# Kernel optimization log

Measured on AMD Instinct MI355X. Metric: run time of the kernel, lower is better.

## Reference

```python
import jax, jax.numpy as jnp
import numpy as np

INF = 1e10
PROBS_THRESHOLD = 0.7
ALPHA = 3.0
DICE_EPS = 1e-6


def edt2d(mask0):
    """Exact Euclidean distance transform of a 2D slice.
    mask0: [H, W] bool, True where the pixel is background (value == 0).
    Returns per-pixel distance to nearest background pixel (0 on background),
    matching scipy.ndimage.distance_transform_edt on the complementary image.
    Separable decomposition: 1D column pass then min-plus row pass.
    """
    H, W = mask0.shape
    ii = jnp.arange(H, dtype=jnp.float32)
    # column pass: g[i, j] = min_{i': mask0[i', j]} |i - i'|   -> [H, W]
    d_col = jnp.abs(ii[:, None] - ii[None, :])                 # [H(i), H(i')]
    g = jnp.min(jnp.where(mask0[None, :, :], d_col[:, :, None], INF), axis=1)
    jj = jnp.arange(W, dtype=jnp.float32)
    dj2 = (jj[:, None] - jj[None, :]) ** 2                     # [W(j), W(j')]
    # row pass: edt^2[i, j] = min_{j'} g[i, j']^2 + (j - j')^2
    edt2 = jnp.min(g[:, None, :] ** 2 + dj2[None, :, :], axis=2)  # [H, W]
    return jnp.sqrt(edt2)


def _combined_distance(y_threshed):
    """y_threshed: [B, 1, D, H, W] float 0/1. Returns combined clipped EDT map."""
    x = y_threshed[:, 0]                                        # [B, D, H, W]
    B, D, H, W = x.shape
    edt_slices = jax.vmap(jax.vmap(lambda s, v: edt2d(s == v), in_axes=(0, None)),
                          in_axes=(0, None))
    dst = edt_slices(x, 1.0)   # distance_transform_edt(slice): bg where slice==0
    inv = edt_slices(x, 0.0)   # wait: see below
    # scipy edt(img): nonzero pixels -> dist to nearest zero => background mask is img==0
    # so dst uses mask0 = (s == 0); inverted uses mask0 = (1 - s == 0) i.e. (s == 1)
    dst = jax.vmap(jax.vmap(lambda s: edt2d(s == 0.0)))(x)      # [B, D, H, W]
    inv = jax.vmap(jax.vmap(lambda s: edt2d(s == 1.0)))(x)      # [B, D, H, W]
    combined = dst + inv
    # get_glioma_indices: first/last slice containing foreground
    present = jnp.any(x > 0, axis=(2, 3))                       # [B, D]
    first = jnp.argmax(present, axis=1)                         # [B]
    last = D - 1 - jnp.argmax(present[:, ::-1], axis=1)         # [B]
    dvec = jnp.arange(D)
    in_range = (dvec[None, :] >= first[:, None]) & (dvec[None, :] <= last[:, None])
    combined = jnp.where(in_range[:, :, None, None], combined, 0.0)
    # thresh_mode == 'max': thresh_val = max of dst of the LAST processed slice
    dst_last = jax.vmap(lambda d, l: d[l])(dst, last)           # [B, H, W]
    thresh = jnp.max(dst_last, axis=(1, 2))                     # [B]
    combined = jnp.minimum(combined, thresh[:, None, None, None])
    return combined[:, None]                                    # [B, 1, D, H, W]


def dice_coefficient(y_pred, y_true):
    inter = jnp.sum(y_pred * y_true)
    return (2.0 * inter) / (jnp.sum(y_pred) + jnp.sum(y_true) + DICE_EPS)


def reference(y_pred, y_true):
    y_threshed = jax.lax.stop_gradient((y_pred > PROBS_THRESHOLD).astype(jnp.float32))
    combined = _combined_distance(y_threshed)                   # [B, 1, D, H, W]
    mask = y_true > 0
    mean_sel = jnp.sum(jnp.where(mask, combined, 0.0)) / jnp.sum(mask)
    distance_loss = jnp.abs(1.0 - mean_sel)
    dice_loss = 1.0 - dice_coefficient(y_pred, y_true)
    return dice_loss + ALPHA * distance_loss


def setup_inputs() -> dict:
    key = jax.random.key(0)
    k1, k2 = jax.random.split(key)
    B, C, D, H, W = 2, 1, 64, 128, 128
    y_pred = jax.random.uniform(k1, (B, C, D, H, W), dtype=jnp.float32)
    y_true = jax.random.randint(k2, (B, C, D, H, W), 0, 2).astype(jnp.float32)
    return {"y_pred": y_pred, "y_true": y_true}
```

## Files before the change

### kernel.cpp

```cpp
#include <hip/hip_runtime.h>
#include <hip/hip_bf16.h>

#define BATCH 2
#define DEPTH 64
#define HH 128
#define WW 128
#define SLICES (BATCH*DEPTH)
#define SLICE_ELEMS (HH*WW)
#define NELEM (SLICES*SLICE_ELEMS)
#define NV4 (NELEM/4)
#define RBLK 1024

__global__ __launch_bounds__(512) void edt_kernel(const float* __restrict__ y_pred,
        float* __restrict__ combined, float* __restrict__ maxdst)
{
    __shared__ unsigned mm_sh[WW][4];
    __shared__ unsigned tmpF[HH][WW];
    __shared__ unsigned tmpB[HH][WW];
    __shared__ float wred[8];
    int s = blockIdx.x;
    int t = threadIdx.x;
    const float* base = y_pred + (size_t)s * SLICE_ELEMS;

    {
        int col = t & (WW-1);
        int g = t >> 7;
        unsigned accm = 0u;
        #pragma unroll
        for (int ii = 0; ii < 32; ++ii) {
            int r = g*32 + ii;
            accm |= (base[r*WW + col] > 0.7f ? 1u : 0u) << ii;
        }
        mm_sh[col][g] = accm;
    }
    __syncthreads();

    if (t < WW) {
        int dd = 300, di = 300;
        #pragma unroll
        for (int g = 0; g < 4; ++g) {
            unsigned mg = mm_sh[t][g];
            #pragma unroll
            for (int ii = 0; ii < 32; ++ii) {
                int i = g*32 + ii;
                int fg = (mg >> ii) & 1;
                dd = fg ? dd + 1 : 0;
                di = fg ? 0 : di + 1;
                tmpF[i][t] = ((unsigned)di << 16) | (unsigned)dd;
            }
        }
    } else if (t < 2*WW) {
        int c = t - WW;
        int dd = 300, di = 300;
        #pragma unroll
        for (int g = 3; g >= 0; --g) {
            unsigned mg = mm_sh[c][g];
            #pragma unroll
            for (int ii = 31; ii >= 0; --ii) {
                int i = g*32 + ii;
                int fg = (mg >> ii) & 1;
                dd = fg ? dd + 1 : 0;
                di = fg ? 0 : di + 1;
                tmpB[i][c] = ((unsigned)di << 16) | (unsigned)dd;
            }
        }
    }
    __syncthreads();

    {
        unsigned* F = &tmpF[0][0];
        unsigned* B = &tmpB[0][0];
        #pragma unroll
        for (int k = 0; k < 32; ++k) {
            int c = k*512 + t;
            unsigned pf = F[c], pb = B[c];
            int fd = min((int)(pf & 0xFFFFu), (int)(pb & 0xFFFFu));
            int fi = min((int)(pf >> 16),     (int)(pb >> 16));
            unsigned sd = (fd >= 128) ? 0xFFFFu : (unsigned)(fd*fd);
            unsigned si = (fi >= 128) ? 0xFFFFu : (unsigned)(fi*fi);
            F[c] = (si << 16) | sd;
        }
    }
    __syncthreads();

    int j  = t & (WW-1);
    int ri = t >> 7;
    float dmax = 0.0f;
    float* cbase = combined + (size_t)s * SLICE_ELEMS;
    for (int it = 0; it < 32; ++it) {
        int i = it*4 + ri;
        unsigned p = tmpF[i][j];
        unsigned rawd = p & 0xFFFFu, rawi = p >> 16;
        int cfg = (rawi == 0u);
        unsigned rsel = cfg ? rawd : rawi;
        float bd = (rsel == 0xFFFFu) ? 1e20f : (float)rsel;
        for (int r = 1; r < WW; ++r) {
            float r2 = (float)(r*r);
            if (__all(r2 >= bd)) break;
            int jl = j - r, jr = j + r;
            unsigned pl = tmpF[i][jl & (WW-1)];
            unsigned pr = tmpF[i][jr & (WW-1)];
            unsigned sl = cfg ? (pl & 0xFFFFu) : (pl >> 16);
            unsigned sr = cfg ? (pr & 0xFFFFu) : (pr >> 16);
            float gl = (sl == 0xFFFFu) ? 1e20f : (float)sl;
            float gr = (sr == 0xFFFFu) ? 1e20f : (float)sr;
            gl = (jl >= 0) ? gl : 3e38f;
            gr = (jr < WW) ? gr : 3e38f;
            bd = fminf(bd, r2 + fminf(gl, gr));
        }
        float dco = sqrtf(bd);
        cbase[i*WW + j] = dco;
        if (cfg) dmax = fmaxf(dmax, dco);
    }
    for (int off = 32; off > 0; off >>= 1)
        dmax = fmaxf(dmax, __shfl_down(dmax, off));
    if ((t & 63) == 0) wred[t >> 6] = dmax;
    __syncthreads();
    if (t == 0) {
        float mx = 0.0f;
        #pragma unroll
        for (int w = 0; w < 8; ++w) mx = fmaxf(mx, wred[w]);
        maxdst[s] = mx;
    }
}

__global__ __launch_bounds__(256) void reduce_kernel(const float4* __restrict__ yp4,
        const float4* __restrict__ yt4, const float4* __restrict__ cb4,
        const float* __restrict__ maxdst, float* __restrict__ partials)
{
    __shared__ int sh_f[2], sh_l[2];
    __shared__ float sh_t[2];
    int t = threadIdx.x;
    if (t < 128) {
        int b = t >> 6, d = t & 63;
        float mx = maxdst[b*DEPTH + d];
        unsigned long long mask = __ballot(mx > 0.0f);
        int f = 0, l = DEPTH-1;
        if (mask) {
            f = __ffsll(mask) - 1;
            l = 63 - __clzll(mask);
        }
        if (d == 0) { sh_f[b] = f; sh_l[b] = l; }
        if (d == l) sh_t[b] = mx;
    }
    __syncthreads();
    int f0 = sh_f[0], l0 = sh_l[0], f1 = sh_f[1], l1 = sh_l[1];
    float th0 = sh_t[0], th1 = sh_t[1];

    float v0=0.f, v1=0.f, v2=0.f, v3=0.f, v4=0.f;
    #pragma unroll
    for (int k = 0; k < 2; ++k) {
        int i4 = k*RBLK*256 + blockIdx.x*256 + t;
        int idx = i4 << 2;
        int b = idx >> 20;
        int d = (idx >> 14) & (DEPTH-1);
        float4 p = yp4[i4];
        float4 q = yt4[i4];
        float4 cc = cb4[i4];
        bool inr = b ? (d >= f1 && d <= l1) : (d >= f0 && d <= l0);
        float th = b ? th1 : th0;
        float c0 = fminf(inr ? cc.x : 0.0f, th);
        float c1 = fminf(inr ? cc.y : 0.0f, th);
        float c2 = fminf(inr ? cc.z : 0.0f, th);
        float c3 = fminf(inr ? cc.w : 0.0f, th);
        float m0 = (q.x > 0.f) ? 1.f : 0.f;
        float m1 = (q.y > 0.f) ? 1.f : 0.f;
        float m2 = (q.z > 0.f) ? 1.f : 0.f;
        float m3 = (q.w > 0.f) ? 1.f : 0.f;
        v0 += p.x*q.x + p.y*q.y + p.z*q.z + p.w*q.w;
        v1 += p.x + p.y + p.z + p.w;
        v2 += q.x + q.y + q.z + q.w;
        v3 += m0*c0 + m1*c1 + m2*c2 + m3*c3;
        v4 += m0 + m1 + m2 + m3;
    }
    for (int off = 32; off > 0; off >>= 1) {
        v0 += __shfl_down(v0, off);
        v1 += __shfl_down(v1, off);
        v2 += __shfl_down(v2, off);
        v3 += __shfl_down(v3, off);
        v4 += __shfl_down(v4, off);
    }
    __shared__ float wsum[4][5];
    int wv = t >> 6;
    if ((t & 63) == 0) {
        wsum[wv][0]=v0; wsum[wv][1]=v1; wsum[wv][2]=v2; wsum[wv][3]=v3; wsum[wv][4]=v4;
    }
    __syncthreads();
    if (t == 0) {
        #pragma unroll
        for (int qd = 0; qd < 5; ++qd)
            partials[qd*RBLK + blockIdx.x] = wsum[0][qd]+wsum[1][qd]+wsum[2][qd]+wsum[3][qd];
    }
}

__global__ __launch_bounds__(1024) void final_kernel(const float* __restrict__ partials,
                                                     float* __restrict__ out)
{
    int t = threadIdx.x;
    double l0 = (double)partials[0*RBLK + t];
    double l1 = (double)partials[1*RBLK + t];
    double l2 = (double)partials[2*RBLK + t];
    double l3 = (double)partials[3*RBLK + t];
    double l4 = (double)partials[4*RBLK + t];
    for (int off = 32; off > 0; off >>= 1) {
        l0 += __shfl_down(l0, off);
        l1 += __shfl_down(l1, off);
        l2 += __shfl_down(l2, off);
        l3 += __shfl_down(l3, off);
        l4 += __shfl_down(l4, off);
    }
    __shared__ double ds[16][5];
    int wv = t >> 6;
    if ((t & 63) == 0) { ds[wv][0]=l0; ds[wv][1]=l1; ds[wv][2]=l2; ds[wv][3]=l3; ds[wv][4]=l4; }
    __syncthreads();
    if (t == 0) {
        double inter=0, spred=0, strue=0, sel=0, cnt=0;
        for (int w = 0; w < 16; ++w) {
            inter += ds[w][0]; spred += ds[w][1]; strue += ds[w][2];
            sel   += ds[w][3]; cnt   += ds[w][4];
        }
        double dice = 2.0 * inter / (spred + strue + 1e-6);
        double mean_sel = sel / cnt;
        double loss = (1.0 - dice) + 3.0 * fabs(1.0 - mean_sel);
        out[0] = (float)loss;
    }
}

extern "C" void kernel_launch(void* const* d_in, const int* in_sizes, int n_in,
                              void* d_out, int out_size, void* d_ws, size_t ws_size,
                              hipStream_t stream) {
    const float* y_pred = (const float*)d_in[0];
    const float* y_true = (const float*)d_in[1];
    float* out = (float*)d_out;
    char* ws = (char*)d_ws;

    float* maxdst   = (float*)(ws + 128);
    float* partials = (float*)(ws + 2048);
    float* combined = (float*)(ws + 32768);

    edt_kernel<<<SLICES, 512, 0, stream>>>(y_pred, combined, maxdst);
    reduce_kernel<<<RBLK, 256, 0, stream>>>((const float4*)y_pred, (const float4*)y_true,
                                            (const float4*)combined, maxdst, partials);
    final_kernel<<<1, 1024, 0, stream>>>(partials, out);
}
```

Baseline: 96.28 us.

## Split EDT slices across two blocks with bitmask column distances

```diff
diff --git a/kernel.cpp b/kernel.cpp
--- a/kernel.cpp
+++ b/kernel.cpp
@@ -11,74 +11,64 @@
 #define NV4 (NELEM/4)
 #define RBLK 1024
 
-__global__ __launch_bounds__(512) void edt_kernel(const float* __restrict__ y_pred,
+__device__ __forceinline__ int ndist(unsigned long long lo, unsigned long long hi, int i) {
+    unsigned long long alo, ahi;
+    if (i < 64) { alo = lo & (~0ull << i); ahi = hi; }
+    else        { alo = 0ull;              ahi = hi & (~0ull << (i - 64)); }
+    int down = alo ? (__ffsll((unsigned long long)alo) - 1 - i)
+                   : (ahi ? (64 + __ffsll((unsigned long long)ahi) - 1 - i) : 1000);
+    unsigned long long blo, bhi;
+    if (i < 64) { blo = (i == 63) ? lo : (lo & ((1ull << (i + 1)) - 1)); bhi = 0ull; }
+    else        { blo = lo; bhi = (i == 127) ? hi : (hi & ((1ull << (i - 63)) - 1)); }
+    int up = bhi ? (i - (127 - __clzll(bhi)))
+                 : (blo ? (i - (63 - __clzll(blo))) : 1000);
+    return min(down, up);
+}
+
+__global__ __launch_bounds__(256) void edt_kernel(const float* __restrict__ y_pred,
         float* __restrict__ combined, float* __restrict__ maxdst)
 {
-    __shared__ unsigned mm_sh[WW][4];
-    __shared__ unsigned tmpF[HH][WW];
-    __shared__ unsigned tmpB[HH][WW];
-    __shared__ float wred[8];
-    int s = blockIdx.x;
-    int t = threadIdx.x;
+    __shared__ unsigned mm_sh[WW][5];
+    __shared__ unsigned tmp[64][WW];
+    __shared__ float wred[4];
+    int blk = blockIdx.x;
+    int s  = blk >> 1;
+    int hb = blk & 1;
+    int t  = threadIdx.x;
     const float* base = y_pred + (size_t)s * SLICE_ELEMS;
 
     {
         int col = t & (WW-1);
-        int g = t >> 7;
-        unsigned accm = 0u;
+        int g0 = (t >> 7) * 2;
+        #pragma unroll
+        for (int k = 0; k < 2; ++k) {
+            int g = g0 + k;
+            unsigned accm = 0u;
+            #pragma unroll
+            for (int ii = 0; ii < 32; ++ii) {
+                int r = g*32 + ii;
+                accm |= (base[r*WW + col] > 0.7f ? 1u : 0u) << ii;
+            }
+            mm_sh[col][g] = accm;
+        }
+    }
+    __syncthreads();
+
+    {
+        int col = t & (WW-1);
+        int rg  = t >> 7;
+        unsigned long long lo = ((unsigned long long)mm_sh[col][1] << 32) | mm_sh[col][0];
+        unsigned long long hi = ((unsigned long long)mm_sh[col][3] << 32) | mm_sh[col][2];
+        unsigned long long nlo = ~lo, nhi = ~hi;
+        int ibase = hb*64 + rg*32;
         #pragma unroll
         for (int ii = 0; ii < 32; ++ii) {
-            int r = g*32 + ii;
-            accm |= (base[r*WW + col] > 0.7f ? 1u : 0u) << ii;
-        }
-        mm_sh[col][g] = accm;
-    }
-    __syncthreads();
-
-    if (t < WW) {
-        int dd = 300, di = 300;
-        #pragma unroll
-        for (int g = 0; g < 4; ++g) {
-            unsigned mg = mm_sh[t][g];
-            #pragma unroll
-            for (int ii = 0; ii < 32; ++ii) {
-                int i = g*32 + ii;
-                int fg = (mg >> ii) & 1;
-                dd = fg ? dd + 1 : 0;
-                di = fg ? 0 : di + 1;
-                tmpF[i][t] = ((unsigned)di << 16) | (unsigned)dd;
-            }
-        }
-    } else if (t < 2*WW) {
-        int c = t - WW;
-        int dd = 300, di = 300;
-        #pragma unroll
-        for (int g = 3; g >= 0; --g) {
-            unsigned mg = mm_sh[c][g];
-            #pragma unroll
-            for (int ii = 31; ii >= 0; --ii) {
-                int i = g*32 + ii;
-                int fg = (mg >> ii) & 1;
-                dd = fg ? dd + 1 : 0;
-                di = fg ? 0 : di + 1;
-                tmpB[i][c] = ((unsigned)di << 16) | (unsigned)dd;
-            }
-        }
-    }
-    __syncthreads();
-
-    {
-        unsigned* F = &tmpF[0][0];
-        unsigned* B = &tmpB[0][0];
-        #pragma unroll
-        for (int k = 0; k < 32; ++k) {
-            int c = k*512 + t;
-            unsigned pf = F[c], pb = B[c];
-            int fd = min((int)(pf & 0xFFFFu), (int)(pb & 0xFFFFu));
-            int fi = min((int)(pf >> 16),     (int)(pb >> 16));
-            unsigned sd = (fd >= 128) ? 0xFFFFu : (unsigned)(fd*fd);
-            unsigned si = (fi >= 128) ? 0xFFFFu : (unsigned)(fi*fi);
-            F[c] = (si << 16) | sd;
+            int i  = ibase + ii;
+            int dd = ndist(nlo, nhi, i);
+            int di = ndist(lo,  hi,  i);
+            unsigned sd = (dd >= 128) ? 0xFFFFu : (unsigned)(dd*dd);
+            unsigned si = (di >= 128) ? 0xFFFFu : (unsigned)(di*di);
+            tmp[rg*32 + ii][col] = (si << 16) | sd;
         }
     }
     __syncthreads();
@@ -88,8 +78,8 @@
     float dmax = 0.0f;
     float* cbase = combined + (size_t)s * SLICE_ELEMS;
     for (int it = 0; it < 32; ++it) {
-        int i = it*4 + ri;
-        unsigned p = tmpF[i][j];
+        int li = it*2 + ri;
+        unsigned p = tmp[li][j];
         unsigned rawd = p & 0xFFFFu, rawi = p >> 16;
         int cfg = (rawi == 0u);
         unsigned rsel = cfg ? rawd : rawi;
@@ -98,8 +88,8 @@
             float r2 = (float)(r*r);
             if (__all(r2 >= bd)) break;
             int jl = j - r, jr = j + r;
-            unsigned pl = tmpF[i][jl & (WW-1)];
-            unsigned pr = tmpF[i][jr & (WW-1)];
+            unsigned pl = tmp[li][jl & (WW-1)];
+            unsigned pr = tmp[li][jr & (WW-1)];
             unsigned sl = cfg ? (pl & 0xFFFFu) : (pl >> 16);
             unsigned sr = cfg ? (pr & 0xFFFFu) : (pr >> 16);
             float gl = (sl == 0xFFFFu) ? 1e20f : (float)sl;
@@ -109,19 +99,15 @@
             bd = fminf(bd, r2 + fminf(gl, gr));
         }
         float dco = sqrtf(bd);
-        cbase[i*WW + j] = dco;
+        cbase[(hb*64 + li)*WW + j] = dco;
         if (cfg) dmax = fmaxf(dmax, dco);
     }
     for (int off = 32; off > 0; off >>= 1)
         dmax = fmaxf(dmax, __shfl_down(dmax, off));
     if ((t & 63) == 0) wred[t >> 6] = dmax;
     __syncthreads();
-    if (t == 0) {
-        float mx = 0.0f;
-        #pragma unroll
-        for (int w = 0; w < 8; ++w) mx = fmaxf(mx, wred[w]);
-        maxdst[s] = mx;
-    }
+    if (t == 0)
+        maxdst[s*2 + hb] = fmaxf(fmaxf(wred[0], wred[1]), fmaxf(wred[2], wred[3]));
 }
 
 __global__ __launch_bounds__(256) void reduce_kernel(const float4* __restrict__ yp4,
@@ -133,7 +119,8 @@
     int t = threadIdx.x;
     if (t < 128) {
         int b = t >> 6, d = t & 63;
-        float mx = maxdst[b*DEPTH + d];
+        int s = b*DEPTH + d;
+        float mx = fmaxf(maxdst[2*s], maxdst[2*s + 1]);
         unsigned long long mask = __ballot(mx > 0.0f);
         int f = 0, l = DEPTH-1;
         if (mask) {
@@ -238,7 +225,7 @@
     float* partials = (float*)(ws + 2048);
     float* combined = (float*)(ws + 32768);
 
-    edt_kernel<<<SLICES, 512, 0, stream>>>(y_pred, combined, maxdst);
+    edt_kernel<<<SLICES*2, 256, 0, stream>>>(y_pred, combined, maxdst);
     reduce_kernel<<<RBLK, 256, 0, stream>>>((const float4*)y_pred, (const float4*)y_true,
                                             (const float4*)combined, maxdst, partials);
     final_kernel<<<1, 1024, 0, stream>>>(partials, out);
```

Measured after the change: 104.5 us. 1.09x slower.
